# Kernel optimization log

Hardware: AMD Instinct MI355X
Metric: run time of the kernel (lower is better)

Reference implementation:

```python
import jax, jax.numpy as jnp
import numpy as np


def setup_inputs() -> dict:
    key = jax.random.key(0)
    k_x, k1, k2, k3 = jax.random.split(key, 4)
    dim, hidden, out_dim = 4096, 8192, 4096
    x = jax.random.normal(k_x, (4, 2048, dim), dtype=jnp.float32)
    # VNNILinear initializes weight = randn(out, in) * 0.02
    w1 = jax.random.normal(k1, (hidden, dim), dtype=jnp.float32) * 0.02
    w2 = jax.random.normal(k2, (out_dim, hidden), dtype=jnp.float32) * 0.02
    w3 = jax.random.normal(k3, (hidden, dim), dtype=jnp.float32) * 0.02
    return {"x": x, "w1": w1, "w2": w2, "w3": w3}


def _quant_linear(x, w):
    """Emulate VNNILinear int8 weight-quantized matmul (inference path).

    Per-output-channel symmetric quant: scale = max|w_row| / 127,
    w_q = round(w / scale) in int8, y = x @ (w_q * scale).T.
    """
    w_max = jnp.clip(jnp.max(jnp.abs(w), axis=1, keepdims=True), 1e-6)  # [out,1]
    scale_w = w_max / 127.0
    w_q = jnp.round(w / scale_w).astype(jnp.int8)
    w_dq = w_q.astype(jnp.float32) * scale_w  # dequantized weight
    return jnp.einsum('bsd,hd->bsh', x, w_dq)


def reference(x, w1, w2, w3):
    # SwiGLU: w2( silu(w1(x)) * w3(x) ), all bias-free, int8 VNNI weight quant
    h = jax.nn.silu(_quant_linear(x, w1)) * _quant_linear(x, w3)  # [B,S,hidden]
    return _quant_linear(h, w2)  # [B,S,out_dim]
```

## Files before the change

kernel.cpp:

```cpp
#include <hip/hip_runtime.h>
#include <hip/hip_bf16.h>
#include <stdint.h>


typedef short bf16x8 __attribute__((ext_vector_type(8)));
typedef float f32x4  __attribute__((ext_vector_type(4)));
typedef float f32x16 __attribute__((ext_vector_type(16)));
typedef int   i32x4  __attribute__((ext_vector_type(4)));
typedef int   i32x16 __attribute__((ext_vector_type(16)));

__device__ __forceinline__ unsigned short f2bf(float f) {
  unsigned u = __builtin_bit_cast(unsigned, f);
  u += 0x7FFFu + ((u >> 16) & 1u);
  return (unsigned short)(u >> 16);
}

#define GLOAD_LDS16(gaddr, laddr)                                             \
  __builtin_amdgcn_global_load_lds(                                           \
      (const __attribute__((address_space(1))) void*)(gaddr),                 \
      (__attribute__((address_space(3))) void*)(laddr), 16, 0, 0)

#define FENCE()      asm volatile("" ::: "memory")
#define BAR()        __builtin_amdgcn_s_barrier()
#define WAIT_LGKM0() asm volatile("s_waitcnt lgkmcnt(0)" ::: "memory")
#define WAIT_LGKM6() asm volatile("s_waitcnt lgkmcnt(6)" ::: "memory")
#define WAIT_VM8()   asm volatile("s_waitcnt vmcnt(8)" ::: "memory")
#define WAIT_VM4()   asm volatile("s_waitcnt vmcnt(4)" ::: "memory")
#define WAIT_VM0()   asm volatile("s_waitcnt vmcnt(0)" ::: "memory")
#define SFENCE()     __builtin_amdgcn_sched_barrier(0)


__global__ void quant_rows_i8_kernel(const float* __restrict__ w,
                                     char* __restrict__ q,
                                     float* __restrict__ scale, int cols,
                                     float clip) {
  const int row = blockIdx.x;
  const float* wr = w + (size_t)row * cols;
  char* qr = q + (size_t)row * cols;

  float m = 0.f;
  for (int c = threadIdx.x * 4; c < cols; c += blockDim.x * 4) {
    float4 v = *reinterpret_cast<const float4*>(wr + c);
    m = fmaxf(m, fmaxf(fmaxf(fabsf(v.x), fabsf(v.y)),
                       fmaxf(fabsf(v.z), fabsf(v.w))));
  }
#pragma unroll
  for (int off = 32; off; off >>= 1) m = fmaxf(m, __shfl_xor(m, off));
  __shared__ float smax[4];
  if ((threadIdx.x & 63) == 0) smax[threadIdx.x >> 6] = m;
  __syncthreads();
  m = fmaxf(fmaxf(smax[0], smax[1]), fmaxf(smax[2], smax[3]));

  const float s = fmaxf(m, clip) / 127.0f;
  if (threadIdx.x == 0) scale[row] = s;
  for (int c = threadIdx.x * 4; c < cols; c += blockDim.x * 4) {
    float4 v = *reinterpret_cast<const float4*>(wr + c);
    int b0 = (int)rintf(v.x / s), b1 = (int)rintf(v.y / s);
    int b2 = (int)rintf(v.z / s), b3 = (int)rintf(v.w / s);
    unsigned pk = (b0 & 0xff) | ((b1 & 0xff) << 8) | ((b2 & 0xff) << 16)
                  | ((b3 & 0xff) << 24);
    *reinterpret_cast<unsigned*>(qr + c) = pk;
  }
}

__global__ void quant_rows_bf16_kernel(const float* __restrict__ w,
                                       unsigned short* __restrict__ wq,
                                       int cols) {
  const int row = blockIdx.x;
  const float* wr = w + (size_t)row * cols;
  unsigned short* wqr = wq + (size_t)row * cols;

  float m = 0.f;
  for (int c = threadIdx.x * 4; c < cols; c += blockDim.x * 4) {
    float4 v = *reinterpret_cast<const float4*>(wr + c);
    m = fmaxf(m, fmaxf(fmaxf(fabsf(v.x), fabsf(v.y)),
                       fmaxf(fabsf(v.z), fabsf(v.w))));
  }
#pragma unroll
  for (int off = 32; off; off >>= 1) m = fmaxf(m, __shfl_xor(m, off));
  __shared__ float smax[4];
  if ((threadIdx.x & 63) == 0) smax[threadIdx.x >> 6] = m;
  __syncthreads();
  m = fmaxf(fmaxf(smax[0], smax[1]), fmaxf(smax[2], smax[3]));

  const float s = fmaxf(m, 1e-6f) / 127.0f;
  for (int c = threadIdx.x * 4; c < cols; c += blockDim.x * 4) {
    float4 v = *reinterpret_cast<const float4*>(wr + c);
    ushort4 o;
    o.x = f2bf(rintf(v.x / s) * s);
    o.y = f2bf(rintf(v.y / s) * s);
    o.z = f2bf(rintf(v.z / s) * s);
    o.w = f2bf(rintf(v.w / s) * s);
    *reinterpret_cast<ushort4*>(wqr + c) = o;
  }
}


__device__ __forceinline__ void xcd_swizzle(int& bx, int& by, int gx, int gy) {
  int nwg = gx * gy;
  int bid = by * gx + bx;
  int cpx = nwg >> 3;
  int s = (bid & 7) * cpx + (bid >> 3);
  by = s / gx;
  bx = s % gx;
}

__global__ __launch_bounds__(512, 2)
void gemm_i8_swiglu_kernel(const char* __restrict__ Aq,
                           const char* __restrict__ B1q,
                           const char* __restrict__ B3q,
                           const float* __restrict__ sx,
                           const float* __restrict__ sw1,
                           const float* __restrict__ sw3,
                           unsigned short* __restrict__ H,
                           int M, int N, int K) {
  __shared__ alignas(1024) char lds[131072];

  int bx = blockIdx.x, by = blockIdx.y;
  xcd_swizzle(bx, by, gridDim.x, gridDim.y);
  const int brow = by * 256, bcol = bx * 128;

  const int t = threadIdx.x, lane = t & 63, w = t >> 6;
  const int wr = w >> 2, wc = w & 3;
  const int l31 = lane & 31, hi = lane >> 5;
  const int NT = K >> 6;

  const int rS = t >> 2;
  const int gcS = ((t & 3) ^ ((t >> 3) & 3)) * 16;
  const char* srcA  = Aq  + (size_t)(brow + rS) * K + gcS;
  const char* srcB1 = B1q + (size_t)(bcol + rS) * K + gcS;
  const char* srcB3 = B3q + (size_t)(bcol + rS) * K + gcS;

#define STAGE_A(kt)                                                           \
  {                                                                           \
    const int s2 = ((kt) & 3) * 32768;                                        \
    const size_t ko = (size_t)(kt) * 64;                                      \
    GLOAD_LDS16(srcA + ko, lds + s2 + t * 16);                                \
    GLOAD_LDS16(srcA + (size_t)128 * K + ko, lds + s2 + 8192 + t * 16);       \
  }
#define STAGE_B(kt)                                                           \
  {                                                                           \
    const int s2 = ((kt) & 3) * 32768;                                        \
    const size_t ko = (size_t)(kt) * 64;                                      \
    GLOAD_LDS16(srcB1 + ko, lds + s2 + 16384 + t * 16);                       \
    GLOAD_LDS16(srcB3 + ko, lds + s2 + 24576 + t * 16);                       \
  }

  STAGE_A(0); STAGE_B(0);
  STAGE_A(1); STAGE_B(1);
  STAGE_A(2); STAGE_B(2);
  WAIT_VM8();
  FENCE(); BAR();

  const int sx2 = (l31 >> 1) & 3;
  const int aoff  = (wr * 128 + l31) * 64 + ((hi ^ sx2) * 16);
  const int boff1 = 16384 + (wc * 32 + l31) * 64 + ((hi ^ sx2) * 16);
  const int boff3 = boff1 + 8192;

  i32x16 acc[4][2] = {};
  i32x4 a0[4], b10, b30;
  i32x4 a1[4], b11, b31;

#pragma unroll
  for (int m = 0; m < 4; ++m)
    a0[m] = *reinterpret_cast<const i32x4*>(lds + aoff + m * 2048);
  b10 = *reinterpret_cast<const i32x4*>(lds + boff1);
  b30 = *reinterpret_cast<const i32x4*>(lds + boff3);

  for (int k = 0; k < NT; ++k) {
    const char* sl = lds + (k & 3) * 32768;
    const bool pf = (k + 3 < NT);

#pragma unroll
    for (int m = 0; m < 4; ++m)
      a1[m] = *reinterpret_cast<const i32x4*>(sl + (aoff ^ 32) + m * 2048);
    b11 = *reinterpret_cast<const i32x4*>(sl + (boff1 ^ 32));
    b31 = *reinterpret_cast<const i32x4*>(sl + (boff3 ^ 32));
    if (pf) STAGE_A(k + 3);
    WAIT_LGKM6();
    SFENCE();
    __builtin_amdgcn_s_setprio(1);
#pragma unroll
    for (int m = 0; m < 4; ++m) {
      acc[m][0] = __builtin_amdgcn_mfma_i32_32x32x32_i8(a0[m], b10,
                                                        acc[m][0], 0, 0, 0);
      acc[m][1] = __builtin_amdgcn_mfma_i32_32x32x32_i8(a0[m], b30,
                                                        acc[m][1], 0, 0, 0);
    }
    __builtin_amdgcn_s_setprio(0);

    if (pf) {
      STAGE_B(k + 3);
      WAIT_VM8();
    } else if (k == NT - 3) {
      WAIT_VM4();
    } else {
      WAIT_VM0();
    }
    WAIT_LGKM0();
    FENCE(); BAR();
    if (k + 1 < NT) {
      const char* sn = lds + ((k + 1) & 3) * 32768;
#pragma unroll
      for (int m = 0; m < 4; ++m)
        a0[m] = *reinterpret_cast<const i32x4*>(sn + aoff + m * 2048);
      b10 = *reinterpret_cast<const i32x4*>(sn + boff1);
      b30 = *reinterpret_cast<const i32x4*>(sn + boff3);
    }
    SFENCE();
    __builtin_amdgcn_s_setprio(1);
#pragma unroll
    for (int m = 0; m < 4; ++m) {
      acc[m][0] = __builtin_amdgcn_mfma_i32_32x32x32_i8(a1[m], b11,
                                                        acc[m][0], 0, 0, 0);
      acc[m][1] = __builtin_amdgcn_mfma_i32_32x32x32_i8(a1[m], b31,
                                                        acc[m][1], 0, 0, 0);
    }
    __builtin_amdgcn_s_setprio(0);
  }
#undef STAGE_A
#undef STAGE_B

  const int ocol = bcol + wc * 32 + l31;
  const int rowb = brow + wr * 128 + 4 * hi;
  const float sw1c = sw1[ocol], sw3c = sw3[ocol];
#pragma unroll
  for (int m = 0; m < 4; ++m) {
#pragma unroll
    for (int rq = 0; rq < 4; ++rq) {
      const int r0 = rowb + m * 32 + 8 * rq;
      const f32x4 sx4 = *reinterpret_cast<const f32x4*>(sx + r0);
#pragma unroll
      for (int j = 0; j < 4; ++j) {
        float y1 = (float)acc[m][0][rq * 4 + j] * (sx4[j] * sw1c);
        float y3 = (float)acc[m][1][rq * 4 + j] * (sx4[j] * sw3c);
        float hv = (y1 / (1.f + __expf(-y1))) * y3;
        H[(size_t)(r0 + j) * N + ocol] = f2bf(hv);
      }
    }
  }
}

__global__ __launch_bounds__(512, 2)
void gemm_bf16_kernel(const unsigned short* __restrict__ A,
                      const unsigned short* __restrict__ B,
                      float* __restrict__ C, int M, int N, int K) {
  __shared__ alignas(1024) unsigned short lds[65536];

  int bx = blockIdx.x, by = blockIdx.y;
  xcd_swizzle(bx, by, gridDim.x, gridDim.y);
  const int brow = by * 256, bcol = bx * 256;

  const int t = threadIdx.x, lane = t & 63, w = t >> 6;
  const int wr = w >> 2, wc = w & 3;
  const int l31 = lane & 31, hi = lane >> 5;
  const int NT = K >> 5;

  const int rS = t >> 2;
  const int cS = ((t & 3) ^ ((t >> 3) & 3)) * 8;
  const unsigned short* srcA = A + (size_t)(brow + rS) * K + cS;
  const unsigned short* srcB = B + (size_t)(bcol + rS) * K + cS;

#define STAGE_A(kt)                                                           \
  {                                                                           \
    const int s2 = ((kt) & 3) * 16384;                                        \
    const size_t ko = (size_t)(kt) * 32;                                      \
    GLOAD_LDS16(srcA + ko, &lds[s2 + t * 8]);                                 \
    GLOAD_LDS16(srcA + (size_t)128 * K + ko, &lds[s2 + 4096 + t * 8]);        \
  }
#define STAGE_B(kt)                                                           \
  {                                                                           \
    const int s2 = ((kt) & 3) * 16384;                                        \
    const size_t ko = (size_t)(kt) * 32;                                      \
    GLOAD_LDS16(srcB + ko, &lds[s2 + 8192 + t * 8]);                          \
    GLOAD_LDS16(srcB + (size_t)128 * K + ko, &lds[s2 + 12288 + t * 8]);       \
  }

  STAGE_A(0); STAGE_B(0);
  STAGE_A(1); STAGE_B(1);
  STAGE_A(2); STAGE_B(2);
  WAIT_VM8();
  FENCE(); BAR();

  const int sx2 = (l31 >> 1) & 3;
  const int aoff  = (wr * 128 + l31) * 32 + ((hi ^ sx2) * 8);
  const int boff0 = 8192 + (wc * 64 + l31) * 32 + ((hi ^ sx2) * 8);

  f32x16 acc[4][2] = {};
  bf16x8 a0[4], b00, b01;
  bf16x8 a1[4], b10, b11;

#pragma unroll
  for (int m = 0; m < 4; ++m)
    a0[m] = *reinterpret_cast<const bf16x8*>(&lds[aoff + m * 1024]);
  b00 = *reinterpret_cast<const bf16x8*>(&lds[boff0]);
  b01 = *reinterpret_cast<const bf16x8*>(&lds[boff0 + 1024]);

  for (int k = 0; k < NT; ++k) {
    const unsigned short* sl = &lds[(k & 3) * 16384];
    const bool pf = (k + 3 < NT);

#pragma unroll
    for (int m = 0; m < 4; ++m)
      a1[m] = *reinterpret_cast<const bf16x8*>(sl + (aoff ^ 16) + m * 1024);
    b10 = *reinterpret_cast<const bf16x8*>(sl + (boff0 ^ 16));
    b11 = *reinterpret_cast<const bf16x8*>(sl + ((boff0 + 1024) ^ 16));
    if (pf) STAGE_A(k + 3);
    WAIT_LGKM6();
    SFENCE();
    __builtin_amdgcn_s_setprio(1);
#pragma unroll
    for (int m = 0; m < 4; ++m) {
      acc[m][0] = __builtin_amdgcn_mfma_f32_32x32x16_bf16(a0[m], b00,
                                                          acc[m][0], 0, 0, 0);
      acc[m][1] = __builtin_amdgcn_mfma_f32_32x32x16_bf16(a0[m], b01,
                                                          acc[m][1], 0, 0, 0);
    }
    __builtin_amdgcn_s_setprio(0);

    if (pf) {
      STAGE_B(k + 3);
      WAIT_VM8();
    } else if (k == NT - 3) {
      WAIT_VM4();
    } else {
      WAIT_VM0();
    }
    WAIT_LGKM0();
    FENCE(); BAR();
    if (k + 1 < NT) {
      const unsigned short* sn = &lds[((k + 1) & 3) * 16384];
#pragma unroll
      for (int m = 0; m < 4; ++m)
        a0[m] = *reinterpret_cast<const bf16x8*>(sn + aoff + m * 1024);
      b00 = *reinterpret_cast<const bf16x8*>(sn + boff0);
      b01 = *reinterpret_cast<const bf16x8*>(sn + boff0 + 1024);
    }
    SFENCE();
    __builtin_amdgcn_s_setprio(1);
#pragma unroll
    for (int m = 0; m < 4; ++m) {
      acc[m][0] = __builtin_amdgcn_mfma_f32_32x32x16_bf16(a1[m], b10,
                                                          acc[m][0], 0, 0, 0);
      acc[m][1] = __builtin_amdgcn_mfma_f32_32x32x16_bf16(a1[m], b11,
                                                          acc[m][1], 0, 0, 0);
    }
    __builtin_amdgcn_s_setprio(0);
  }
#undef STAGE_A
#undef STAGE_B

  const int ocol = bcol + wc * 64 + l31;
  const int rowb = brow + wr * 128 + 4 * hi;
#pragma unroll
  for (int m = 0; m < 4; ++m)
#pragma unroll
    for (int n = 0; n < 2; ++n)
#pragma unroll
      for (int rq = 0; rq < 4; ++rq)
#pragma unroll
        for (int j = 0; j < 4; ++j)
          C[(size_t)(rowb + m * 32 + 8 * rq + j) * N + (ocol + n * 32)] =
              acc[m][n][rq * 4 + j];
}


extern "C" void kernel_launch(void* const* d_in, const int* in_sizes, int n_in,
                              void* d_out, int out_size, void* d_ws,
                              size_t ws_size, hipStream_t stream) {
  const float* x  = (const float*)d_in[0];
  const float* w1 = (const float*)d_in[1];
  const float* w2 = (const float*)d_in[2];
  const float* w3 = (const float*)d_in[3];
  float* out = (float*)d_out;

  const int DIM = 4096, HID = 8192;
  const int M = in_sizes[0] / DIM;

  char* xq  = (char*)d_ws;
  char* w1q = xq + (size_t)M * DIM;
  char* w3q = w1q + (size_t)HID * DIM;
  unsigned short* w2b = (unsigned short*)(w3q + (size_t)HID * DIM);
  unsigned short* h = w2b + (size_t)DIM * HID;
  float* sx  = (float*)(h + (size_t)M * HID);
  float* sw1 = sx + M;
  float* sw3 = sw1 + HID;

  quant_rows_i8_kernel<<<HID, 256, 0, stream>>>(w1, w1q, sw1, DIM, 1e-6f);
  quant_rows_i8_kernel<<<HID, 256, 0, stream>>>(w3, w3q, sw3, DIM, 1e-6f);
  quant_rows_i8_kernel<<<M, 256, 0, stream>>>(x, xq, sx, DIM, 1e-30f);
  quant_rows_bf16_kernel<<<DIM, 256, 0, stream>>>(w2, w2b, HID);

  gemm_i8_swiglu_kernel<<<dim3(HID / 128, M / 256), 512, 0, stream>>>(
      xq, w1q, w3q, sx, sw1, sw3, h, M, HID, DIM);
  gemm_bf16_kernel<<<dim3(DIM / 256, M / 256), 512, 0, stream>>>(
      h, w2b, out, M, DIM, HID);
}
```

Baseline: 1.244 ms.

## Interleave LDS fragment loads with MFMA groups inside each k-tile

Both GEMM main loops drop the cross-iteration register double-buffering of A/B fragments. Each tile's fragments are now loaded in four smaller LDS batches, each followed by four MFMAs guarded by finer lgkmcnt waits, with the global prefetches placed between them. The aim is to cut register pressure and hide LDS latency within the tile. The trade-off is that the first loads of each tile are no longer prefetched before the barrier, so part of the LDS latency now sits on the critical path after every barrier.

New measurement: 1.307 ms. 1.05x slower.

```diff
diff --git a/kernel.cpp b/kernel.cpp
--- a/kernel.cpp
+++ b/kernel.cpp
@@ -22,12 +22,13 @@
 
 #define FENCE()      asm volatile("" ::: "memory")
 #define BAR()        __builtin_amdgcn_s_barrier()
-#define WAIT_LGKM0() asm volatile("s_waitcnt lgkmcnt(0)" ::: "memory")
-#define WAIT_LGKM6() asm volatile("s_waitcnt lgkmcnt(6)" ::: "memory")
+#define WAIT_LGKM(n) asm volatile("s_waitcnt lgkmcnt(" #n ")" ::: "memory")
 #define WAIT_VM8()   asm volatile("s_waitcnt vmcnt(8)" ::: "memory")
 #define WAIT_VM4()   asm volatile("s_waitcnt vmcnt(4)" ::: "memory")
 #define WAIT_VM0()   asm volatile("s_waitcnt vmcnt(0)" ::: "memory")
 #define SFENCE()     __builtin_amdgcn_sched_barrier(0)
+#define PRIO1()      __builtin_amdgcn_s_setprio(1)
+#define PRIO0()      __builtin_amdgcn_s_setprio(0)
 
 
 __global__ void quant_rows_i8_kernel(const float* __restrict__ w,
@@ -158,65 +159,66 @@
   const int boff3 = boff1 + 8192;
 
   i32x16 acc[4][2] = {};
-  i32x4 a0[4], b10, b30;
-  i32x4 a1[4], b11, b31;
-
-#pragma unroll
-  for (int m = 0; m < 4; ++m)
-    a0[m] = *reinterpret_cast<const i32x4*>(lds + aoff + m * 2048);
-  b10 = *reinterpret_cast<const i32x4*>(lds + boff1);
-  b30 = *reinterpret_cast<const i32x4*>(lds + boff3);
 
   for (int k = 0; k < NT; ++k) {
     const char* sl = lds + (k & 3) * 32768;
     const bool pf = (k + 3 < NT);
-
-#pragma unroll
-    for (int m = 0; m < 4; ++m)
-      a1[m] = *reinterpret_cast<const i32x4*>(sl + (aoff ^ 32) + m * 2048);
-    b11 = *reinterpret_cast<const i32x4*>(sl + (boff1 ^ 32));
-    b31 = *reinterpret_cast<const i32x4*>(sl + (boff3 ^ 32));
+    i32x4 a00, a01, a02, a03, b01f, b03f;
+    i32x4 a10, a11, a12, a13, b11f, b13f;
+
+    a00 = *reinterpret_cast<const i32x4*>(sl + aoff);
+    a01 = *reinterpret_cast<const i32x4*>(sl + aoff + 2048);
+    b01f = *reinterpret_cast<const i32x4*>(sl + boff1);
+    b03f = *reinterpret_cast<const i32x4*>(sl + boff3);
+    a02 = *reinterpret_cast<const i32x4*>(sl + aoff + 4096);
+    a03 = *reinterpret_cast<const i32x4*>(sl + aoff + 6144);
     if (pf) STAGE_A(k + 3);
-    WAIT_LGKM6();
-    SFENCE();
-    __builtin_amdgcn_s_setprio(1);
-#pragma unroll
-    for (int m = 0; m < 4; ++m) {
-      acc[m][0] = __builtin_amdgcn_mfma_i32_32x32x32_i8(a0[m], b10,
-                                                        acc[m][0], 0, 0, 0);
-      acc[m][1] = __builtin_amdgcn_mfma_i32_32x32x32_i8(a0[m], b30,
-                                                        acc[m][1], 0, 0, 0);
-    }
-    __builtin_amdgcn_s_setprio(0);
-
+    WAIT_LGKM(2); SFENCE();
+    PRIO1();
+    acc[0][0] = __builtin_amdgcn_mfma_i32_32x32x32_i8(a00, b01f, acc[0][0], 0, 0, 0);
+    acc[0][1] = __builtin_amdgcn_mfma_i32_32x32x32_i8(a00, b03f, acc[0][1], 0, 0, 0);
+    acc[1][0] = __builtin_amdgcn_mfma_i32_32x32x32_i8(a01, b01f, acc[1][0], 0, 0, 0);
+    acc[1][1] = __builtin_amdgcn_mfma_i32_32x32x32_i8(a01, b03f, acc[1][1], 0, 0, 0);
+    PRIO0();
+
+    a10 = *reinterpret_cast<const i32x4*>(sl + (aoff ^ 32));
+    a11 = *reinterpret_cast<const i32x4*>(sl + (aoff ^ 32) + 2048);
+    b11f = *reinterpret_cast<const i32x4*>(sl + (boff1 ^ 32));
+    b13f = *reinterpret_cast<const i32x4*>(sl + (boff3 ^ 32));
+    WAIT_LGKM(4); SFENCE();
+    PRIO1();
+    acc[2][0] = __builtin_amdgcn_mfma_i32_32x32x32_i8(a02, b01f, acc[2][0], 0, 0, 0);
+    acc[2][1] = __builtin_amdgcn_mfma_i32_32x32x32_i8(a02, b03f, acc[2][1], 0, 0, 0);
+    acc[3][0] = __builtin_amdgcn_mfma_i32_32x32x32_i8(a03, b01f, acc[3][0], 0, 0, 0);
+    acc[3][1] = __builtin_amdgcn_mfma_i32_32x32x32_i8(a03, b03f, acc[3][1], 0, 0, 0);
+    PRIO0();
+
+    a12 = *reinterpret_cast<const i32x4*>(sl + (aoff ^ 32) + 4096);
+    a13 = *reinterpret_cast<const i32x4*>(sl + (aoff ^ 32) + 6144);
+    if (pf) STAGE_B(k + 3);
+    WAIT_LGKM(2); SFENCE();
+    PRIO1();
+    acc[0][0] = __builtin_amdgcn_mfma_i32_32x32x32_i8(a10, b11f, acc[0][0], 0, 0, 0);
+    acc[0][1] = __builtin_amdgcn_mfma_i32_32x32x32_i8(a10, b13f, acc[0][1], 0, 0, 0);
+    acc[1][0] = __builtin_amdgcn_mfma_i32_32x32x32_i8(a11, b11f, acc[1][0], 0, 0, 0);
+    acc[1][1] = __builtin_amdgcn_mfma_i32_32x32x32_i8(a11, b13f, acc[1][1], 0, 0, 0);
+    PRIO0();
+
+    WAIT_LGKM(0); SFENCE();
+    PRIO1();
+    acc[2][0] = __builtin_amdgcn_mfma_i32_32x32x32_i8(a12, b11f, acc[2][0], 0, 0, 0);
+    acc[2][1] = __builtin_amdgcn_mfma_i32_32x32x32_i8(a12, b13f, acc[2][1], 0, 0, 0);
+    acc[3][0] = __builtin_amdgcn_mfma_i32_32x32x32_i8(a13, b11f, acc[3][0], 0, 0, 0);
+    acc[3][1] = __builtin_amdgcn_mfma_i32_32x32x32_i8(a13, b13f, acc[3][1], 0, 0, 0);
+    PRIO0();
     if (pf) {
-      STAGE_B(k + 3);
       WAIT_VM8();
     } else if (k == NT - 3) {
       WAIT_VM4();
-    } else {
+    } else if (k == NT - 2) {
       WAIT_VM0();
     }
-    WAIT_LGKM0();
     FENCE(); BAR();
-    if (k + 1 < NT) {
-      const char* sn = lds + ((k + 1) & 3) * 32768;
-#pragma unroll
-      for (int m = 0; m < 4; ++m)
-        a0[m] = *reinterpret_cast<const i32x4*>(sn + aoff + m * 2048);
-      b10 = *reinterpret_cast<const i32x4*>(sn + boff1);
-      b30 = *reinterpret_cast<const i32x4*>(sn + boff3);
-    }
-    SFENCE();
-    __builtin_amdgcn_s_setprio(1);
-#pragma unroll
-    for (int m = 0; m < 4; ++m) {
-      acc[m][0] = __builtin_amdgcn_mfma_i32_32x32x32_i8(a1[m], b11,
-                                                        acc[m][0], 0, 0, 0);
-      acc[m][1] = __builtin_amdgcn_mfma_i32_32x32x32_i8(a1[m], b31,
-                                                        acc[m][1], 0, 0, 0);
-    }
-    __builtin_amdgcn_s_setprio(0);
   }
 #undef STAGE_A
 #undef STAGE_B
@@ -287,65 +289,66 @@
   const int boff0 = 8192 + (wc * 64 + l31) * 32 + ((hi ^ sx2) * 8);
 
   f32x16 acc[4][2] = {};
-  bf16x8 a0[4], b00, b01;
-  bf16x8 a1[4], b10, b11;
-
-#pragma unroll
-  for (int m = 0; m < 4; ++m)
-    a0[m] = *reinterpret_cast<const bf16x8*>(&lds[aoff + m * 1024]);
-  b00 = *reinterpret_cast<const bf16x8*>(&lds[boff0]);
-  b01 = *reinterpret_cast<const bf16x8*>(&lds[boff0 + 1024]);
 
   for (int k = 0; k < NT; ++k) {
     const unsigned short* sl = &lds[(k & 3) * 16384];
     const bool pf = (k + 3 < NT);
-
-#pragma unroll
-    for (int m = 0; m < 4; ++m)
-      a1[m] = *reinterpret_cast<const bf16x8*>(sl + (aoff ^ 16) + m * 1024);
+    bf16x8 a00, a01, a02, a03, b00, b01;
+    bf16x8 a10, a11, a12, a13, b10, b11;
+
+    a00 = *reinterpret_cast<const bf16x8*>(sl + aoff);
+    a01 = *reinterpret_cast<const bf16x8*>(sl + aoff + 1024);
+    b00 = *reinterpret_cast<const bf16x8*>(sl + boff0);
+    b01 = *reinterpret_cast<const bf16x8*>(sl + boff0 + 1024);
+    a02 = *reinterpret_cast<const bf16x8*>(sl + aoff + 2048);
+    a03 = *reinterpret_cast<const bf16x8*>(sl + aoff + 3072);
+    if (pf) STAGE_A(k + 3);
+    WAIT_LGKM(2); SFENCE();
+    PRIO1();
+    acc[0][0] = __builtin_amdgcn_mfma_f32_32x32x16_bf16(a00, b00, acc[0][0], 0, 0, 0);
+    acc[0][1] = __builtin_amdgcn_mfma_f32_32x32x16_bf16(a00, b01, acc[0][1], 0, 0, 0);
+    acc[1][0] = __builtin_amdgcn_mfma_f32_32x32x16_bf16(a01, b00, acc[1][0], 0, 0, 0);
+    acc[1][1] = __builtin_amdgcn_mfma_f32_32x32x16_bf16(a01, b01, acc[1][1], 0, 0, 0);
+    PRIO0();
+
+    a10 = *reinterpret_cast<const bf16x8*>(sl + (aoff ^ 16));
+    a11 = *reinterpret_cast<const bf16x8*>(sl + (aoff ^ 16) + 1024);
     b10 = *reinterpret_cast<const bf16x8*>(sl + (boff0 ^ 16));
     b11 = *reinterpret_cast<const bf16x8*>(sl + ((boff0 + 1024) ^ 16));
-    if (pf) STAGE_A(k + 3);
-    WAIT_LGKM6();
-    SFENCE();
-    __builtin_amdgcn_s_setprio(1);
-#pragma unroll
-    for (int m = 0; m < 4; ++m) {
-      acc[m][0] = __builtin_amdgcn_mfma_f32_32x32x16_bf16(a0[m], b00,
-                                                          acc[m][0], 0, 0, 0);
-      acc[m][1] = __builtin_amdgcn_mfma_f32_32x32x16_bf16(a0[m], b01,
-                                                          acc[m][1], 0, 0, 0);
-    }
-    __builtin_amdgcn_s_setprio(0);
-
+    WAIT_LGKM(4); SFENCE();
+    PRIO1();
+    acc[2][0] = __builtin_amdgcn_mfma_f32_32x32x16_bf16(a02, b00, acc[2][0], 0, 0, 0);
+    acc[2][1] = __builtin_amdgcn_mfma_f32_32x32x16_bf16(a02, b01, acc[2][1], 0, 0, 0);
+    acc[3][0] = __builtin_amdgcn_mfma_f32_32x32x16_bf16(a03, b00, acc[3][0], 0, 0, 0);
+    acc[3][1] = __builtin_amdgcn_mfma_f32_32x32x16_bf16(a03, b01, acc[3][1], 0, 0, 0);
+    PRIO0();
+
+    a12 = *reinterpret_cast<const bf16x8*>(sl + (aoff ^ 16) + 2048);
+    a13 = *reinterpret_cast<const bf16x8*>(sl + (aoff ^ 16) + 3072);
+    if (pf) STAGE_B(k + 3);
+    WAIT_LGKM(2); SFENCE();
+    PRIO1();
+    acc[0][0] = __builtin_amdgcn_mfma_f32_32x32x16_bf16(a10, b10, acc[0][0], 0, 0, 0);
+    acc[0][1] = __builtin_amdgcn_mfma_f32_32x32x16_bf16(a10, b11, acc[0][1], 0, 0, 0);
+    acc[1][0] = __builtin_amdgcn_mfma_f32_32x32x16_bf16(a11, b10, acc[1][0], 0, 0, 0);
+    acc[1][1] = __builtin_amdgcn_mfma_f32_32x32x16_bf16(a11, b11, acc[1][1], 0, 0, 0);
+    PRIO0();
+
+    WAIT_LGKM(0); SFENCE();
+    PRIO1();
+    acc[2][0] = __builtin_amdgcn_mfma_f32_32x32x16_bf16(a12, b10, acc[2][0], 0, 0, 0);
+    acc[2][1] = __builtin_amdgcn_mfma_f32_32x32x16_bf16(a12, b11, acc[2][1], 0, 0, 0);
+    acc[3][0] = __builtin_amdgcn_mfma_f32_32x32x16_bf16(a13, b10, acc[3][0], 0, 0, 0);
+    acc[3][1] = __builtin_amdgcn_mfma_f32_32x32x16_bf16(a13, b11, acc[3][1], 0, 0, 0);
+    PRIO0();
     if (pf) {
-      STAGE_B(k + 3);
       WAIT_VM8();
     } else if (k == NT - 3) {
       WAIT_VM4();
-    } else {
+    } else if (k == NT - 2) {
       WAIT_VM0();
     }
-    WAIT_LGKM0();
     FENCE(); BAR();
-    if (k + 1 < NT) {
-      const unsigned short* sn = &lds[((k + 1) & 3) * 16384];
-#pragma unroll
-      for (int m = 0; m < 4; ++m)
-        a0[m] = *reinterpret_cast<const bf16x8*>(sn + aoff + m * 1024);
-      b00 = *reinterpret_cast<const bf16x8*>(sn + boff0);
-      b01 = *reinterpret_cast<const bf16x8*>(sn + boff0 + 1024);
-    }
-    SFENCE();
-    __builtin_amdgcn_s_setprio(1);
-#pragma unroll
-    for (int m = 0; m < 4; ++m) {
-      acc[m][0] = __builtin_amdgcn_mfma_f32_32x32x16_bf16(a1[m], b10,
-                                                          acc[m][0], 0, 0, 0);
-      acc[m][1] = __builtin_amdgcn_mfma_f32_32x32x16_bf16(a1[m], b11,
-                                                          acc[m][1], 0, 0, 0);
-    }
-    __builtin_amdgcn_s_setprio(0);
   }
 #undef STAGE_A
 #undef STAGE_B
```

## Restructure GEMM pipelines to two-tile periods and register-cache quant row loads

Applied to the files above, without the earlier changes.

Both GEMM main loops are rewritten to stage two K-tiles at a time into a four-slot LDS ring and synchronise once per pair of tiles, with register double-buffered fragment loads interleaved between MFMA groups. This halves the barrier and vmcnt-wait count per K step. The row-quantization kernels become templated on the column count and keep the row in registers, so each weight row is read from global memory once instead of twice. In exchange the prefetch distance is shorter and each barrier waits on all outstanding loads (vmcnt 0), which could expose memory latency.

New measurement: 1.265 ms. No clear change (+1.7%).

```diff
diff --git a/kernel.cpp b/kernel.cpp
--- a/kernel.cpp
+++ b/kernel.cpp
@@ -22,27 +22,28 @@
 
 #define FENCE()      asm volatile("" ::: "memory")
 #define BAR()        __builtin_amdgcn_s_barrier()
-#define WAIT_LGKM0() asm volatile("s_waitcnt lgkmcnt(0)" ::: "memory")
-#define WAIT_LGKM6() asm volatile("s_waitcnt lgkmcnt(6)" ::: "memory")
-#define WAIT_VM8()   asm volatile("s_waitcnt vmcnt(8)" ::: "memory")
-#define WAIT_VM4()   asm volatile("s_waitcnt vmcnt(4)" ::: "memory")
+#define WAIT_LGKM(n) asm volatile("s_waitcnt lgkmcnt(" #n ")" ::: "memory")
 #define WAIT_VM0()   asm volatile("s_waitcnt vmcnt(0)" ::: "memory")
 #define SFENCE()     __builtin_amdgcn_sched_barrier(0)
-
-
-__global__ void quant_rows_i8_kernel(const float* __restrict__ w,
-                                     char* __restrict__ q,
-                                     float* __restrict__ scale, int cols,
-                                     float clip) {
-  const int row = blockIdx.x;
-  const float* wr = w + (size_t)row * cols;
-  char* qr = q + (size_t)row * cols;
-
+#define PRIO1()      __builtin_amdgcn_s_setprio(1)
+#define PRIO0()      __builtin_amdgcn_s_setprio(0)
+
+
+template <int NCH>
+__global__ void quant_rows_i8_sp(const float* __restrict__ w,
+                                 char* __restrict__ q,
+                                 float* __restrict__ scale, float clip) {
+  const int cols = NCH * 1024;
+  const float* wr = w + (size_t)blockIdx.x * cols;
+  char* qr = q + (size_t)blockIdx.x * cols;
+
+  float4 v[NCH];
   float m = 0.f;
-  for (int c = threadIdx.x * 4; c < cols; c += blockDim.x * 4) {
-    float4 v = *reinterpret_cast<const float4*>(wr + c);
-    m = fmaxf(m, fmaxf(fmaxf(fabsf(v.x), fabsf(v.y)),
-                       fmaxf(fabsf(v.z), fabsf(v.w))));
+#pragma unroll
+  for (int j = 0; j < NCH; ++j) {
+    v[j] = *reinterpret_cast<const float4*>(wr + threadIdx.x * 4 + j * 1024);
+    m = fmaxf(m, fmaxf(fmaxf(fabsf(v[j].x), fabsf(v[j].y)),
+                       fmaxf(fabsf(v[j].z), fabsf(v[j].w))));
   }
 #pragma unroll
   for (int off = 32; off; off >>= 1) m = fmaxf(m, __shfl_xor(m, off));
@@ -52,29 +53,31 @@
   m = fmaxf(fmaxf(smax[0], smax[1]), fmaxf(smax[2], smax[3]));
 
   const float s = fmaxf(m, clip) / 127.0f;
-  if (threadIdx.x == 0) scale[row] = s;
-  for (int c = threadIdx.x * 4; c < cols; c += blockDim.x * 4) {
-    float4 v = *reinterpret_cast<const float4*>(wr + c);
-    int b0 = (int)rintf(v.x / s), b1 = (int)rintf(v.y / s);
-    int b2 = (int)rintf(v.z / s), b3 = (int)rintf(v.w / s);
+  if (threadIdx.x == 0) scale[blockIdx.x] = s;
+#pragma unroll
+  for (int j = 0; j < NCH; ++j) {
+    int b0 = (int)rintf(v[j].x / s), b1 = (int)rintf(v[j].y / s);
+    int b2 = (int)rintf(v[j].z / s), b3 = (int)rintf(v[j].w / s);
     unsigned pk = (b0 & 0xff) | ((b1 & 0xff) << 8) | ((b2 & 0xff) << 16)
                   | ((b3 & 0xff) << 24);
-    *reinterpret_cast<unsigned*>(qr + c) = pk;
-  }
-}
-
-__global__ void quant_rows_bf16_kernel(const float* __restrict__ w,
-                                       unsigned short* __restrict__ wq,
-                                       int cols) {
-  const int row = blockIdx.x;
-  const float* wr = w + (size_t)row * cols;
-  unsigned short* wqr = wq + (size_t)row * cols;
-
+    *reinterpret_cast<unsigned*>(qr + threadIdx.x * 4 + j * 1024) = pk;
+  }
+}
+
+template <int NCH>
+__global__ void quant_rows_bf16_sp(const float* __restrict__ w,
+                                   unsigned short* __restrict__ wq) {
+  const int cols = NCH * 1024;
+  const float* wr = w + (size_t)blockIdx.x * cols;
+  unsigned short* wqr = wq + (size_t)blockIdx.x * cols;
+
+  float4 v[NCH];
   float m = 0.f;
-  for (int c = threadIdx.x * 4; c < cols; c += blockDim.x * 4) {
-    float4 v = *reinterpret_cast<const float4*>(wr + c);
-    m = fmaxf(m, fmaxf(fmaxf(fabsf(v.x), fabsf(v.y)),
-                       fmaxf(fabsf(v.z), fabsf(v.w))));
+#pragma unroll
+  for (int j = 0; j < NCH; ++j) {
+    v[j] = *reinterpret_cast<const float4*>(wr + threadIdx.x * 4 + j * 1024);
+    m = fmaxf(m, fmaxf(fmaxf(fabsf(v[j].x), fabsf(v[j].y)),
+                       fmaxf(fabsf(v[j].z), fabsf(v[j].w))));
   }
 #pragma unroll
   for (int off = 32; off; off >>= 1) m = fmaxf(m, __shfl_xor(m, off));
@@ -84,14 +87,14 @@
   m = fmaxf(fmaxf(smax[0], smax[1]), fmaxf(smax[2], smax[3]));
 
   const float s = fmaxf(m, 1e-6f) / 127.0f;
-  for (int c = threadIdx.x * 4; c < cols; c += blockDim.x * 4) {
-    float4 v = *reinterpret_cast<const float4*>(wr + c);
+#pragma unroll
+  for (int j = 0; j < NCH; ++j) {
     ushort4 o;
-    o.x = f2bf(rintf(v.x / s) * s);
-    o.y = f2bf(rintf(v.y / s) * s);
-    o.z = f2bf(rintf(v.z / s) * s);
-    o.w = f2bf(rintf(v.w / s) * s);
-    *reinterpret_cast<ushort4*>(wqr + c) = o;
+    o.x = f2bf(rintf(v[j].x / s) * s);
+    o.y = f2bf(rintf(v[j].y / s) * s);
+    o.z = f2bf(rintf(v[j].z / s) * s);
+    o.w = f2bf(rintf(v[j].w / s) * s);
+    *reinterpret_cast<ushort4*>(wqr + threadIdx.x * 4 + j * 1024) = o;
   }
 }
 
@@ -131,95 +134,96 @@
   const char* srcB1 = B1q + (size_t)(bcol + rS) * K + gcS;
   const char* srcB3 = B3q + (size_t)(bcol + rS) * K + gcS;
 
-#define STAGE_A(kt)                                                           \
+#define STAGE_FT(sp, kt)                                                      \
   {                                                                           \
-    const int s2 = ((kt) & 3) * 32768;                                        \
     const size_t ko = (size_t)(kt) * 64;                                      \
-    GLOAD_LDS16(srcA + ko, lds + s2 + t * 16);                                \
-    GLOAD_LDS16(srcA + (size_t)128 * K + ko, lds + s2 + 8192 + t * 16);       \
-  }
-#define STAGE_B(kt)                                                           \
-  {                                                                           \
-    const int s2 = ((kt) & 3) * 32768;                                        \
-    const size_t ko = (size_t)(kt) * 64;                                      \
-    GLOAD_LDS16(srcB1 + ko, lds + s2 + 16384 + t * 16);                       \
-    GLOAD_LDS16(srcB3 + ko, lds + s2 + 24576 + t * 16);                       \
-  }
-
-  STAGE_A(0); STAGE_B(0);
-  STAGE_A(1); STAGE_B(1);
-  STAGE_A(2); STAGE_B(2);
-  WAIT_VM8();
-  FENCE(); BAR();
+    GLOAD_LDS16(srcA + ko, (sp) + t * 16);                                    \
+    GLOAD_LDS16(srcA + (size_t)128 * K + ko, (sp) + 8192 + t * 16);           \
+    GLOAD_LDS16(srcB1 + ko, (sp) + 16384 + t * 16);                          \
+    GLOAD_LDS16(srcB3 + ko, (sp) + 24576 + t * 16);                          \
+  }
 
   const int sx2 = (l31 >> 1) & 3;
   const int aoff  = (wr * 128 + l31) * 64 + ((hi ^ sx2) * 16);
   const int boff1 = 16384 + (wc * 32 + l31) * 64 + ((hi ^ sx2) * 16);
   const int boff3 = boff1 + 8192;
 
+#define LOADSET_F(aa, bb1, bb3, base, xr)                                     \
+  aa[0] = *reinterpret_cast<const i32x4*>((base) + (aoff ^ (xr)));            \
+  aa[1] = *reinterpret_cast<const i32x4*>((base) + (aoff ^ (xr)) + 2048);     \
+  aa[2] = *reinterpret_cast<const i32x4*>((base) + (aoff ^ (xr)) + 4096);     \
+  aa[3] = *reinterpret_cast<const i32x4*>((base) + (aoff ^ (xr)) + 6144);     \
+  bb1 = *reinterpret_cast<const i32x4*>((base) + (boff1 ^ (xr)));             \
+  bb3 = *reinterpret_cast<const i32x4*>((base) + (boff3 ^ (xr)));
+
   i32x16 acc[4][2] = {};
   i32x4 a0[4], b10, b30;
   i32x4 a1[4], b11, b31;
 
-#pragma unroll
-  for (int m = 0; m < 4; ++m)
-    a0[m] = *reinterpret_cast<const i32x4*>(lds + aoff + m * 2048);
-  b10 = *reinterpret_cast<const i32x4*>(lds + boff1);
-  b30 = *reinterpret_cast<const i32x4*>(lds + boff3);
-
-  for (int k = 0; k < NT; ++k) {
-    const char* sl = lds + (k & 3) * 32768;
-    const bool pf = (k + 3 < NT);
-
-#pragma unroll
-    for (int m = 0; m < 4; ++m)
-      a1[m] = *reinterpret_cast<const i32x4*>(sl + (aoff ^ 32) + m * 2048);
-    b11 = *reinterpret_cast<const i32x4*>(sl + (boff1 ^ 32));
-    b31 = *reinterpret_cast<const i32x4*>(sl + (boff3 ^ 32));
-    if (pf) STAGE_A(k + 3);
-    WAIT_LGKM6();
-    SFENCE();
-    __builtin_amdgcn_s_setprio(1);
-#pragma unroll
-    for (int m = 0; m < 4; ++m) {
-      acc[m][0] = __builtin_amdgcn_mfma_i32_32x32x32_i8(a0[m], b10,
-                                                        acc[m][0], 0, 0, 0);
-      acc[m][1] = __builtin_amdgcn_mfma_i32_32x32x32_i8(a0[m], b30,
-                                                        acc[m][1], 0, 0, 0);
+#define MFMA8_F(ar, b1r, b3r)                                                 \
+  acc[0][0] = __builtin_amdgcn_mfma_i32_32x32x32_i8(ar[0], b1r, acc[0][0], 0, 0, 0); \
+  acc[0][1] = __builtin_amdgcn_mfma_i32_32x32x32_i8(ar[0], b3r, acc[0][1], 0, 0, 0); \
+  acc[1][0] = __builtin_amdgcn_mfma_i32_32x32x32_i8(ar[1], b1r, acc[1][0], 0, 0, 0); \
+  acc[1][1] = __builtin_amdgcn_mfma_i32_32x32x32_i8(ar[1], b3r, acc[1][1], 0, 0, 0); \
+  acc[2][0] = __builtin_amdgcn_mfma_i32_32x32x32_i8(ar[2], b1r, acc[2][0], 0, 0, 0); \
+  acc[2][1] = __builtin_amdgcn_mfma_i32_32x32x32_i8(ar[2], b3r, acc[2][1], 0, 0, 0); \
+  acc[3][0] = __builtin_amdgcn_mfma_i32_32x32x32_i8(ar[3], b1r, acc[3][0], 0, 0, 0); \
+  acc[3][1] = __builtin_amdgcn_mfma_i32_32x32x32_i8(ar[3], b3r, acc[3][1], 0, 0, 0)
+
+#define PERIOD_CORE_F(S0, S1)                                                 \
+  WAIT_LGKM(6); SFENCE();                                                     \
+  PRIO1(); MFMA8_F(a0, b10, b30); PRIO0();                                    \
+  LOADSET_F(a0, b10, b30, (S1), 0);                                           \
+  WAIT_LGKM(6); SFENCE();                                                     \
+  PRIO1(); MFMA8_F(a1, b11, b31); PRIO0();                                    \
+  LOADSET_F(a1, b11, b31, (S1), 32);                                          \
+  WAIT_LGKM(6); SFENCE();                                                     \
+  PRIO1(); MFMA8_F(a0, b10, b30); PRIO0();                                    \
+  WAIT_LGKM(0); WAIT_VM0(); FENCE(); BAR();
+
+  STAGE_FT(lds, 0);
+  STAGE_FT(lds + 32768, 1);
+  WAIT_VM0(); FENCE(); BAR();
+  LOADSET_F(a0, b10, b30, lds, 0);
+
+  int kb = 0;
+  for (; kb + 6 <= NT; kb += 4) {
+    LOADSET_F(a1, b11, b31, lds, 32);
+    STAGE_FT(lds + 65536, kb + 2);
+    STAGE_FT(lds + 98304, kb + 3);
+    PERIOD_CORE_F(lds, lds + 32768);
+    LOADSET_F(a0, b10, b30, lds + 65536, 0);
+    SFENCE();
+    PRIO1(); MFMA8_F(a1, b11, b31); PRIO0();
+
+    LOADSET_F(a1, b11, b31, lds + 65536, 32);
+    STAGE_FT(lds, kb + 4);
+    STAGE_FT(lds + 32768, kb + 5);
+    PERIOD_CORE_F(lds + 65536, lds + 98304);
+    LOADSET_F(a0, b10, b30, lds, 0);
+    SFENCE();
+    PRIO1(); MFMA8_F(a1, b11, b31); PRIO0();
+  }
+
+  for (int t0 = kb; t0 < NT; t0 += 2) {
+    const char* s0p = lds + (t0 & 3) * 32768;
+    const char* s1p = lds + ((t0 + 1) & 3) * 32768;
+    LOADSET_F(a1, b11, b31, s0p, 32);
+    if (t0 + 3 < NT) {
+      STAGE_FT(lds + ((t0 + 2) & 3) * 32768, t0 + 2);
+      STAGE_FT(lds + ((t0 + 3) & 3) * 32768, t0 + 3);
     }
-    __builtin_amdgcn_s_setprio(0);
-
-    if (pf) {
-      STAGE_B(k + 3);
-      WAIT_VM8();
-    } else if (k == NT - 3) {
-      WAIT_VM4();
-    } else {
-      WAIT_VM0();
+    PERIOD_CORE_F(s0p, s1p);
+    if (t0 + 2 < NT) {
+      LOADSET_F(a0, b10, b30, lds + ((t0 + 2) & 3) * 32768, 0);
     }
-    WAIT_LGKM0();
-    FENCE(); BAR();
-    if (k + 1 < NT) {
-      const char* sn = lds + ((k + 1) & 3) * 32768;
-#pragma unroll
-      for (int m = 0; m < 4; ++m)
-        a0[m] = *reinterpret_cast<const i32x4*>(sn + aoff + m * 2048);
-      b10 = *reinterpret_cast<const i32x4*>(sn + boff1);
-      b30 = *reinterpret_cast<const i32x4*>(sn + boff3);
-    }
-    SFENCE();
-    __builtin_amdgcn_s_setprio(1);
-#pragma unroll
-    for (int m = 0; m < 4; ++m) {
-      acc[m][0] = __builtin_amdgcn_mfma_i32_32x32x32_i8(a1[m], b11,
-                                                        acc[m][0], 0, 0, 0);
-      acc[m][1] = __builtin_amdgcn_mfma_i32_32x32x32_i8(a1[m], b31,
-                                                        acc[m][1], 0, 0, 0);
-    }
-    __builtin_amdgcn_s_setprio(0);
-  }
-#undef STAGE_A
-#undef STAGE_B
+    SFENCE();
+    PRIO1(); MFMA8_F(a1, b11, b31); PRIO0();
+  }
+#undef PERIOD_CORE_F
+#undef MFMA8_F
+#undef LOADSET_F
+#undef STAGE_FT
 
   const int ocol = bcol + wc * 32 + l31;
   const int rowb = brow + wr * 128 + 4 * hi;
@@ -261,94 +265,96 @@
   const unsigned short* srcA = A + (size_t)(brow + rS) * K + cS;
   const unsigned short* srcB = B + (size_t)(bcol + rS) * K + cS;
 
-#define STAGE_A(kt)                                                           \
+#define STAGE_GT(sp, kt)                                                      \
   {                                                                           \
-    const int s2 = ((kt) & 3) * 16384;                                        \
     const size_t ko = (size_t)(kt) * 32;                                      \
-    GLOAD_LDS16(srcA + ko, &lds[s2 + t * 8]);                                 \
-    GLOAD_LDS16(srcA + (size_t)128 * K + ko, &lds[s2 + 4096 + t * 8]);        \
-  }
-#define STAGE_B(kt)                                                           \
-  {                                                                           \
-    const int s2 = ((kt) & 3) * 16384;                                        \
-    const size_t ko = (size_t)(kt) * 32;                                      \
-    GLOAD_LDS16(srcB + ko, &lds[s2 + 8192 + t * 8]);                          \
-    GLOAD_LDS16(srcB + (size_t)128 * K + ko, &lds[s2 + 12288 + t * 8]);       \
-  }
-
-  STAGE_A(0); STAGE_B(0);
-  STAGE_A(1); STAGE_B(1);
-  STAGE_A(2); STAGE_B(2);
-  WAIT_VM8();
-  FENCE(); BAR();
+    GLOAD_LDS16(srcA + ko, (sp) + t * 8);                                     \
+    GLOAD_LDS16(srcA + (size_t)128 * K + ko, (sp) + 4096 + t * 8);            \
+    GLOAD_LDS16(srcB + ko, (sp) + 8192 + t * 8);                              \
+    GLOAD_LDS16(srcB + (size_t)128 * K + ko, (sp) + 12288 + t * 8);           \
+  }
 
   const int sx2 = (l31 >> 1) & 3;
   const int aoff  = (wr * 128 + l31) * 32 + ((hi ^ sx2) * 8);
   const int boff0 = 8192 + (wc * 64 + l31) * 32 + ((hi ^ sx2) * 8);
+  const int boff1b = boff0 + 1024;
+
+#define LOADSET_G(aa, bb0, bb1, base, xr)                                     \
+  aa[0] = *reinterpret_cast<const bf16x8*>((base) + (aoff ^ (xr)));           \
+  aa[1] = *reinterpret_cast<const bf16x8*>((base) + (aoff ^ (xr)) + 1024);    \
+  aa[2] = *reinterpret_cast<const bf16x8*>((base) + (aoff ^ (xr)) + 2048);    \
+  aa[3] = *reinterpret_cast<const bf16x8*>((base) + (aoff ^ (xr)) + 3072);    \
+  bb0 = *reinterpret_cast<const bf16x8*>((base) + (boff0 ^ (xr)));            \
+  bb1 = *reinterpret_cast<const bf16x8*>((base) + (boff1b ^ (xr)));
 
   f32x16 acc[4][2] = {};
   bf16x8 a0[4], b00, b01;
   bf16x8 a1[4], b10, b11;
 
-#pragma unroll
-  for (int m = 0; m < 4; ++m)
-    a0[m] = *reinterpret_cast<const bf16x8*>(&lds[aoff + m * 1024]);
-  b00 = *reinterpret_cast<const bf16x8*>(&lds[boff0]);
-  b01 = *reinterpret_cast<const bf16x8*>(&lds[boff0 + 1024]);
-
-  for (int k = 0; k < NT; ++k) {
-    const unsigned short* sl = &lds[(k & 3) * 16384];
-    const bool pf = (k + 3 < NT);
-
-#pragma unroll
-    for (int m = 0; m < 4; ++m)
-      a1[m] = *reinterpret_cast<const bf16x8*>(sl + (aoff ^ 16) + m * 1024);
-    b10 = *reinterpret_cast<const bf16x8*>(sl + (boff0 ^ 16));
-    b11 = *reinterpret_cast<const bf16x8*>(sl + ((boff0 + 1024) ^ 16));
-    if (pf) STAGE_A(k + 3);
-    WAIT_LGKM6();
-    SFENCE();
-    __builtin_amdgcn_s_setprio(1);
-#pragma unroll
-    for (int m = 0; m < 4; ++m) {
-      acc[m][0] = __builtin_amdgcn_mfma_f32_32x32x16_bf16(a0[m], b00,
-                                                          acc[m][0], 0, 0, 0);
-      acc[m][1] = __builtin_amdgcn_mfma_f32_32x32x16_bf16(a0[m], b01,
-                                                          acc[m][1], 0, 0, 0);
+#define MFMA8_G(ar, bx0, bx1)                                                 \
+  acc[0][0] = __builtin_amdgcn_mfma_f32_32x32x16_bf16(ar[0], bx0, acc[0][0], 0, 0, 0); \
+  acc[0][1] = __builtin_amdgcn_mfma_f32_32x32x16_bf16(ar[0], bx1, acc[0][1], 0, 0, 0); \
+  acc[1][0] = __builtin_amdgcn_mfma_f32_32x32x16_bf16(ar[1], bx0, acc[1][0], 0, 0, 0); \
+  acc[1][1] = __builtin_amdgcn_mfma_f32_32x32x16_bf16(ar[1], bx1, acc[1][1], 0, 0, 0); \
+  acc[2][0] = __builtin_amdgcn_mfma_f32_32x32x16_bf16(ar[2], bx0, acc[2][0], 0, 0, 0); \
+  acc[2][1] = __builtin_amdgcn_mfma_f32_32x32x16_bf16(ar[2], bx1, acc[2][1], 0, 0, 0); \
+  acc[3][0] = __builtin_amdgcn_mfma_f32_32x32x16_bf16(ar[3], bx0, acc[3][0], 0, 0, 0); \
+  acc[3][1] = __builtin_amdgcn_mfma_f32_32x32x16_bf16(ar[3], bx1, acc[3][1], 0, 0, 0)
+
+#define PERIOD_CORE_G(S0, S1)                                                 \
+  WAIT_LGKM(6); SFENCE();                                                     \
+  PRIO1(); MFMA8_G(a0, b00, b01); PRIO0();                                    \
+  LOADSET_G(a0, b00, b01, (S1), 0);                                           \
+  WAIT_LGKM(6); SFENCE();                                                     \
+  PRIO1(); MFMA8_G(a1, b10, b11); PRIO0();                                    \
+  LOADSET_G(a1, b10, b11, (S1), 16);                                          \
+  WAIT_LGKM(6); SFENCE();                                                     \
+  PRIO1(); MFMA8_G(a0, b00, b01); PRIO0();                                    \
+  WAIT_LGKM(0); WAIT_VM0(); FENCE(); BAR();
+
+  STAGE_GT(lds, 0);
+  STAGE_GT(lds + 16384, 1);
+  WAIT_VM0(); FENCE(); BAR();
+  LOADSET_G(a0, b00, b01, lds, 0);
+
+  int kb = 0;
+  for (; kb + 6 <= NT; kb += 4) {
+    LOADSET_G(a1, b10, b11, lds, 16);
+    STAGE_GT(lds + 32768, kb + 2);
+    STAGE_GT(lds + 49152, kb + 3);
+    PERIOD_CORE_G(lds, lds + 16384);
+    LOADSET_G(a0, b00, b01, lds + 32768, 0);
+    SFENCE();
+    PRIO1(); MFMA8_G(a1, b10, b11); PRIO0();
+
+    LOADSET_G(a1, b10, b11, lds + 32768, 16);
+    STAGE_GT(lds, kb + 4);
+    STAGE_GT(lds + 16384, kb + 5);
+    PERIOD_CORE_G(lds + 32768, lds + 49152);
+    LOADSET_G(a0, b00, b01, lds, 0);
+    SFENCE();
+    PRIO1(); MFMA8_G(a1, b10, b11); PRIO0();
+  }
+
+  for (int t0 = kb; t0 < NT; t0 += 2) {
+    const unsigned short* s0p = lds + (t0 & 3) * 16384;
+    const unsigned short* s1p = lds + ((t0 + 1) & 3) * 16384;
+    LOADSET_G(a1, b10, b11, s0p, 16);
+    if (t0 + 3 < NT) {
+      STAGE_GT(lds + ((t0 + 2) & 3) * 16384, t0 + 2);
+      STAGE_GT(lds + ((t0 + 3) & 3) * 16384, t0 + 3);
     }
-    __builtin_amdgcn_s_setprio(0);
-
-    if (pf) {
-      STAGE_B(k + 3);
-      WAIT_VM8();
-    } else if (k == NT - 3) {
-      WAIT_VM4();
-    } else {
-      WAIT_VM0();
+    PERIOD_CORE_G(s0p, s1p);
+    if (t0 + 2 < NT) {
+      LOADSET_G(a0, b00, b01, lds + ((t0 + 2) & 3) * 16384, 0);
     }
-    WAIT_LGKM0();
-    FENCE(); BAR();
-    if (k + 1 < NT) {
-      const unsigned short* sn = &lds[((k + 1) & 3) * 16384];
-#pragma unroll
-      for (int m = 0; m < 4; ++m)
-        a0[m] = *reinterpret_cast<const bf16x8*>(sn + aoff + m * 1024);
-      b00 = *reinterpret_cast<const bf16x8*>(sn + boff0);
-      b01 = *reinterpret_cast<const bf16x8*>(sn + boff0 + 1024);
-    }
-    SFENCE();
-    __builtin_amdgcn_s_setprio(1);
-#pragma unroll
-    for (int m = 0; m < 4; ++m) {
-      acc[m][0] = __builtin_amdgcn_mfma_f32_32x32x16_bf16(a1[m], b10,
-                                                          acc[m][0], 0, 0, 0);
-      acc[m][1] = __builtin_amdgcn_mfma_f32_32x32x16_bf16(a1[m], b11,
-                                                          acc[m][1], 0, 0, 0);
-    }
-    __builtin_amdgcn_s_setprio(0);
-  }
-#undef STAGE_A
-#undef STAGE_B
+    SFENCE();
+    PRIO1(); MFMA8_G(a1, b10, b11); PRIO0();
+  }
+#undef PERIOD_CORE_G
+#undef MFMA8_G
+#undef LOADSET_G
+#undef STAGE_GT
 
   const int ocol = bcol + wc * 64 + l31;
   const int rowb = brow + wr * 128 + 4 * hi;
@@ -386,10 +392,10 @@
   float* sw1 = sx + M;
   float* sw3 = sw1 + HID;
 
-  quant_rows_i8_kernel<<<HID, 256, 0, stream>>>(w1, w1q, sw1, DIM, 1e-6f);
-  quant_rows_i8_kernel<<<HID, 256, 0, stream>>>(w3, w3q, sw3, DIM, 1e-6f);
-  quant_rows_i8_kernel<<<M, 256, 0, stream>>>(x, xq, sx, DIM, 1e-30f);
-  quant_rows_bf16_kernel<<<DIM, 256, 0, stream>>>(w2, w2b, HID);
+  quant_rows_i8_sp<4><<<HID, 256, 0, stream>>>(w1, w1q, sw1, 1e-6f);
+  quant_rows_i8_sp<4><<<HID, 256, 0, stream>>>(w3, w3q, sw3, 1e-6f);
+  quant_rows_i8_sp<4><<<M, 256, 0, stream>>>(x, xq, sx, 1e-30f);
+  quant_rows_bf16_sp<8><<<DIM, 256, 0, stream>>>(w2, w2b);
 
   gemm_i8_swiglu_kernel<<<dim3(HID / 128, M / 256), 512, 0, stream>>>(
       xq, w1q, w3q, sx, sw1, sw3, h, M, HID, DIM);
```
